# Performance work log

Measured on AMD Instinct MI355X. Metric: run time of the kernel, lower is better.

Reference implementation:

```python
import jax, jax.numpy as jnp
import numpy as np

B, S, D, H = 2, 2048, 1024, 16
DK = D // H  # 64


def setup_inputs() -> dict:
    key = jax.random.key(0)
    k0, k1, k2, k3, k4, k5, k6 = jax.random.split(key, 7)
    scale = 0.02
    return {
        "q": jax.random.normal(k0, (B, S, D), dtype=jnp.float32),
        "k": jax.random.normal(k1, (B, S, D), dtype=jnp.float32),
        "v": jax.random.normal(k2, (B, S, D), dtype=jnp.float32),
        # per-head Q/K projection weights (n_head separate Linear layers, bias=False)
        "Wq": jax.random.normal(k3, (H, D, DK), dtype=jnp.float32) * scale,
        "Wk": jax.random.normal(k4, (H, D, DK), dtype=jnp.float32) * scale,
        # shared V projection (the same v_layer object is reused for every head)
        "Wv": jax.random.normal(k5, (D, DK), dtype=jnp.float32) * scale,
        # output projection fc: d_v -> d_model, bias=False
        "Wo": jax.random.normal(k6, (DK, D), dtype=jnp.float32) * scale,
    }


def reference(q, k, v, Wq, Wk, Wv, Wo):
    d_k = Wq.shape[-1]
    # batched per-head projections (replaces the Python loop over heads)
    qs = jnp.einsum("bsd,hdk->bhsk", q, Wq)          # [B,H,S,DK]
    ks = jnp.einsum("bsd,hdk->bhsk", k, Wk)          # [B,H,S,DK]
    vs = jnp.einsum("bsd,dk->bsk", v, Wv)            # [B,S,DK] shared across heads
    scores = jnp.einsum("bhsk,bhtk->bhst", qs, ks) / jnp.sqrt(
        jnp.asarray(d_k, dtype=jnp.float32)
    )                                                 # [B,H,S,S]
    attn = jax.nn.softmax(scores, axis=-1)            # [B,H,S,S]; dropout = identity (eval)
    heads = jnp.einsum("bhst,btk->bhsk", attn, vs)    # [B,H,S,DK]
    head = heads.mean(axis=1)                         # mean over heads, not concat
    attn_mean = attn.mean(axis=1)                     # [B,S,S]
    out = jnp.einsum("bsk,kd->bsd", head, Wo)         # [B,S,D]; dropout = identity
    return (out, attn_mean)
```

## Files before the change

### kernel.cpp

```cpp
#include <hip/hip_runtime.h>

#define B_ 2
#define S_ 2048
#define D_ 1024
#define H_ 16
#define DK_ 64

typedef __bf16 bf8 __attribute__((ext_vector_type(8)));
typedef float f4 __attribute__((ext_vector_type(4)));
typedef unsigned short u16x8 __attribute__((ext_vector_type(8)));

__device__ __forceinline__ unsigned short f2bf_bits(float f) {
  unsigned int u = __float_as_uint(f);
  return (unsigned short)((u + 0x7fffu + ((u >> 16) & 1u)) >> 16);
}

__device__ __forceinline__ bf8 pack_bf8(f4 lo, f4 hi) {
  u16x8 u;
  u[0] = f2bf_bits(lo[0]); u[1] = f2bf_bits(lo[1]);
  u[2] = f2bf_bits(lo[2]); u[3] = f2bf_bits(lo[3]);
  u[4] = f2bf_bits(hi[0]); u[5] = f2bf_bits(hi[1]);
  u[6] = f2bf_bits(hi[2]); u[7] = f2bf_bits(hi[3]);
  union { u16x8 u; bf8 b; } x; x.u = u; return x.b;
}

__device__ __forceinline__ bf8 ldb(const unsigned short* p) {
  return *reinterpret_cast<const bf8*>(p);
}

__device__ __forceinline__ void stage16(const void* g, void* l) {
  __builtin_amdgcn_global_load_lds(
      (const __attribute__((address_space(1))) void*)g,
      (__attribute__((address_space(3))) void*)l, 16, 0, 0);
}

#define MFMA(a, b, c) __builtin_amdgcn_mfma_f32_16x16x32_bf16((a), (b), (c), 0, 0, 0)

__global__ void k_prep(const float* __restrict__ q, const float* __restrict__ k,
                       const float* __restrict__ wq, const float* __restrict__ wk,
                       const float* __restrict__ wv, const float* __restrict__ wo,
                       unsigned short* __restrict__ qb, unsigned short* __restrict__ kb,
                       unsigned short* __restrict__ wqt, unsigned short* __restrict__ wkt,
                       unsigned short* __restrict__ wvt, unsigned short* __restrict__ wot) {
  __shared__ float tl[64 * 65];
  int bid = blockIdx.x, tid = threadIdx.x;
  const int rr = tid >> 6, cc = tid & 63;
  if (bid < 4096) {
    int which = bid >> 11;
    long i = ((long)(bid & 2047) * 256 + tid) * 8;
    const float* src = which ? k : q;
    unsigned short* dst = which ? kb : qb;
    f4 lo = *reinterpret_cast<const f4*>(src + i);
    f4 hi = *reinterpret_cast<const f4*>(src + i + 4);
    *reinterpret_cast<bf8*>(dst + i) = pack_bf8(lo, hi);
  } else if (bid < 4352) {
    int blk = bid - 4096;
    int h = blk >> 4, d0 = (blk & 15) * 64;
    for (int m = 0; m < 2; ++m) {
      const float* src = m ? wk : wq;
      unsigned short* dst = m ? wkt : wqt;
      if (m) __syncthreads();
#pragma unroll
      for (int it = 0; it < 16; ++it) {
        int d = it * 4 + rr;
        tl[cc * 65 + d] = src[(long)h * 65536 + (d0 + d) * 64 + cc];
      }
      __syncthreads();
#pragma unroll
      for (int it = 0; it < 16; ++it) {
        int n = it * 4 + rr;
        dst[(long)h * 65536 + n * 1024 + d0 + cc] = f2bf_bits(tl[n * 65 + cc]);
      }
    }
  } else if (bid < 4368) {
    int d0 = (bid - 4352) * 64;
#pragma unroll
    for (int it = 0; it < 16; ++it) {
      int d = it * 4 + rr;
      tl[cc * 65 + d] = wv[(long)(d0 + d) * 64 + cc];
    }
    __syncthreads();
#pragma unroll
    for (int it = 0; it < 16; ++it) {
      int n = it * 4 + rr;
      wvt[(long)n * 1024 + d0 + cc] = f2bf_bits(tl[n * 65 + cc]);
    }
  } else {
    int d0 = (bid - 4368) * 64;
#pragma unroll
    for (int it = 0; it < 16; ++it) {
      int kk = it * 4 + rr;
      tl[cc * 65 + kk] = wo[(long)kk * 1024 + d0 + cc];
    }
    __syncthreads();
#pragma unroll
    for (int it = 0; it < 16; ++it) {
      int ddl = it * 4 + rr;
      wot[(long)(d0 + ddl) * 64 + cc] = f2bf_bits(tl[ddl * 65 + cc]);
    }
  }
}

__global__ __launch_bounds__(256) void k_gemm_qk(
    const unsigned short* __restrict__ qb, const unsigned short* __restrict__ kb,
    const unsigned short* __restrict__ wqt, const unsigned short* __restrict__ wkt,
    unsigned short* __restrict__ qsb, unsigned short* __restrict__ ksb) {
  __shared__ unsigned short lds[16384];
  const int tid = threadIdx.x, wave = tid >> 6, lane = tid & 63;
  const int l15 = lane & 15, quad = lane >> 4;
  const int m0 = blockIdx.x * 128, n0 = blockIdx.y * 128;
  const int which = blockIdx.z;
  const unsigned short* A = which ? kb : qb;
  const unsigned short* W = which ? wkt : wqt;
  unsigned short* C = which ? ksb : qsb;
  const float scale = which ? 1.0f : 0.18033688011112042f;
  const int wr = wave >> 1, wc = wave & 1;

  f4 acc[4][4];
#pragma unroll
  for (int i = 0; i < 4; ++i)
#pragma unroll
    for (int j = 0; j < 4; ++j) acc[i][j] = f4{0.f, 0.f, 0.f, 0.f};

  for (int k0 = 0; k0 < D_; k0 += 64) {
#pragma unroll
    for (int i = 0; i < 4; ++i) {
      int u = i * 256 + tid;
      int T = u >> 6, rg = T & 7, kh = T >> 3, sl15 = u & 15, squad = (u >> 4) & 3;
      stage16(A + (long)(m0 + rg * 16 + sl15) * D_ + k0 + kh * 32 + squad * 8, lds + u * 8);
      stage16(W + (long)(n0 + rg * 16 + sl15) * D_ + k0 + kh * 32 + squad * 8,
              lds + 8192 + u * 8);
    }
    __syncthreads();
#pragma unroll
    for (int kh = 0; kh < 2; ++kh) {
      bf8 aF[4], bF[4];
#pragma unroll
      for (int mi = 0; mi < 4; ++mi)
        aF[mi] = ldb(lds + (wr * 4 + mi + 8 * kh) * 512 + lane * 8);
#pragma unroll
      for (int ni = 0; ni < 4; ++ni)
        bF[ni] = ldb(lds + 8192 + (wc * 4 + ni + 8 * kh) * 512 + lane * 8);
#pragma unroll
      for (int mi = 0; mi < 4; ++mi)
#pragma unroll
        for (int ni = 0; ni < 4; ++ni)
          acc[mi][ni] = MFMA(aF[mi], bF[ni], acc[mi][ni]);
    }
    __syncthreads();
  }
#pragma unroll
  for (int mi = 0; mi < 4; ++mi)
#pragma unroll
    for (int r = 0; r < 4; ++r) {
      long row = m0 + wr * 64 + mi * 16 + quad * 4 + r;
#pragma unroll
      for (int ni = 0; ni < 4; ++ni)
        C[row * D_ + n0 + wc * 64 + ni * 16 + l15] = f2bf_bits(acc[mi][ni][r] * scale);
    }
}

__global__ __launch_bounds__(256) void k_pv(
    const float* __restrict__ v, const unsigned short* __restrict__ wvt,
    float* __restrict__ pv) {
  const int tid = threadIdx.x, wave = tid >> 6, lane = tid & 63;
  const int l15 = lane & 15, quad = lane >> 4;
  const int rg = blockIdx.x, kc = blockIdx.y;
  const int row0 = rg * 64 + wave * 16;
  const float* arow = v + (long)(row0 + l15) * D_ + kc * 128 + quad * 8;
  const unsigned short* wbase = wvt + kc * 128 + quad * 8;
  f4 acc[4];
  for (int i = 0; i < 4; ++i) acc[i] = f4{0.f, 0.f, 0.f, 0.f};
#pragma unroll
  for (int k0 = 0; k0 < 128; k0 += 32) {
    f4 alo = *reinterpret_cast<const f4*>(arow + k0);
    f4 ahi = *reinterpret_cast<const f4*>(arow + k0 + 4);
    bf8 a = pack_bf8(alo, ahi);
#pragma unroll
    for (int i = 0; i < 4; ++i) {
      bf8 bf = ldb(wbase + (long)(i * 16 + l15) * D_ + k0);
      acc[i] = MFMA(a, bf, acc[i]);
    }
  }
#pragma unroll
  for (int i = 0; i < 4; ++i)
#pragma unroll
    for (int r = 0; r < 4; ++r)
      pv[((long)kc * 4096 + row0 + quad * 4 + r) * 64 + i * 16 + l15] = acc[i][r];
}

__global__ void k_vred(const float* __restrict__ pv, unsigned short* __restrict__ vst) {
  int e = blockIdx.x * 256 + threadIdx.x;
  int t = e & 2047, dk = (e >> 11) & 63, b = e >> 17;
  long row = (long)b * S_ + t;
  float s = 0.f;
#pragma unroll
  for (int c = 0; c < 8; ++c) s += pv[((long)c * 4096 + row) * 64 + dk];
  vst[e] = f2bf_bits(s);
}

__global__ __launch_bounds__(256) void k_denom(
    const unsigned short* __restrict__ qsb, const unsigned short* __restrict__ ksb,
    float* __restrict__ recip) {
  __shared__ unsigned short lds[16384];
  const int tid = threadIdx.x, wave = tid >> 6, lane = tid & 63;
  const int l15 = lane & 15, quad = lane >> 4;
  const int stile = blockIdx.x, h = blockIdx.y, b = blockIdx.z;
  const int sw = stile * 128 + wave * 32;

  const unsigned short* qrow0 = qsb + ((long)(b * S_) + sw + l15) * D_ + h * 64 + quad * 8;
  bf8 a0 = ldb(qrow0);
  bf8 a1 = ldb(qrow0 + 32);
  bf8 a2 = ldb(qrow0 + 16 * D_);
  bf8 a3 = ldb(qrow0 + 16 * D_ + 32);

  f4 sum0 = f4{0.f, 0.f, 0.f, 0.f}, sum1 = f4{0.f, 0.f, 0.f, 0.f};

  const long kbase = (long)(b * S_);
#pragma unroll
  for (int i = 0; i < 4; ++i) {
    int u = i * 256 + tid;
    int T = u >> 6, sl15 = u & 15, squad = (u >> 4) & 3;
    stage16(ksb + (kbase + (T & 7) * 16 + sl15) * D_ + h * 64 + (T >> 3) * 32 + squad * 8,
            lds + u * 8);
  }
  for (int it = 0; it < 16; ++it) {
    __syncthreads();
    if (it < 15) {
      int t0n = (it + 1) * 128, bufn = (it + 1) & 1;
#pragma unroll
      for (int i = 0; i < 4; ++i) {
        int u = i * 256 + tid;
        int T = u >> 6, sl15 = u & 15, squad = (u >> 4) & 3;
        stage16(ksb + (kbase + t0n + (T & 7) * 16 + sl15) * D_ + h * 64 + (T >> 3) * 32 + squad * 8,
                lds + bufn * 8192 + u * 8);
      }
    }
    const unsigned short* L = lds + (it & 1) * 8192;
#pragma unroll
    for (int tt = 0; tt < 8; ++tt) {
      bf8 b0 = ldb(L + tt * 512 + lane * 8);
      bf8 b1 = ldb(L + 4096 + tt * 512 + lane * 8);
      f4 d0 = f4{0.f, 0.f, 0.f, 0.f};
      d0 = MFMA(a0, b0, d0);
      d0 = MFMA(a1, b1, d0);
      f4 d1 = f4{0.f, 0.f, 0.f, 0.f};
      d1 = MFMA(a2, b0, d1);
      d1 = MFMA(a3, b1, d1);
#pragma unroll
      for (int r = 0; r < 4; ++r) {
        sum0[r] += __builtin_amdgcn_exp2f(d0[r]);
        sum1[r] += __builtin_amdgcn_exp2f(d1[r]);
      }
    }
  }
#pragma unroll
  for (int m = 1; m < 16; m <<= 1) {
#pragma unroll
    for (int r = 0; r < 4; ++r) {
      sum0[r] += __shfl_xor(sum0[r], m, 64);
      sum1[r] += __shfl_xor(sum1[r], m, 64);
    }
  }
  if (l15 == 0) {
    float* rp0 = recip + (long)(b * H_ + h) * S_ + sw + quad * 4;
#pragma unroll
    for (int r = 0; r < 4; ++r) {
      rp0[r] = 1.0f / (16.0f * sum0[r]);
      rp0[16 + r] = 1.0f / (16.0f * sum1[r]);
    }
  }
}

__global__ __launch_bounds__(256) void k_attn(
    const unsigned short* __restrict__ qsb, const unsigned short* __restrict__ ksb,
    const float* __restrict__ recip, float* __restrict__ am) {
  __shared__ unsigned short lds[16384];
  const int tid = threadIdx.x, wave = tid >> 6, lane = tid & 63;
  const int l15 = lane & 15, quad = lane >> 4;
  const int tchunk = blockIdx.x, stile = blockIdx.y, b = blockIdx.z;
  const int sw = stile * 128 + wave * 32;
  const int t0c = tchunk * 128;

  f4 acc0[8], acc1[8];
#pragma unroll
  for (int tt = 0; tt < 8; ++tt) {
    acc0[tt] = f4{0.f, 0.f, 0.f, 0.f};
    acc1[tt] = f4{0.f, 0.f, 0.f, 0.f};
  }

  const unsigned short* qrow0 = qsb + ((long)(b * S_) + sw + l15) * D_ + quad * 8;
  const long kbase = (long)(b * S_) + t0c;

#pragma unroll
  for (int i = 0; i < 4; ++i) {
    int u = i * 256 + tid;
    int T = u >> 6, sl15 = u & 15, squad = (u >> 4) & 3;
    stage16(ksb + (kbase + (T & 7) * 16 + sl15) * D_ + (T >> 3) * 32 + squad * 8, lds + u * 8);
  }
  for (int h = 0; h < H_; ++h) {
    __syncthreads();
    if (h < 15) {
      int bufn = (h + 1) & 1;
#pragma unroll
      for (int i = 0; i < 4; ++i) {
        int u = i * 256 + tid;
        int T = u >> 6, sl15 = u & 15, squad = (u >> 4) & 3;
        stage16(ksb + (kbase + (T & 7) * 16 + sl15) * D_ + (h + 1) * 64 + (T >> 3) * 32 + squad * 8,
                lds + bufn * 8192 + u * 8);
      }
    }
    const unsigned short* L = lds + (h & 1) * 8192;
    bf8 a0 = ldb(qrow0 + h * 64);
    bf8 a1 = ldb(qrow0 + h * 64 + 32);
    bf8 a2 = ldb(qrow0 + 16 * D_ + h * 64);
    bf8 a3 = ldb(qrow0 + 16 * D_ + h * 64 + 32);
    const float* rpp = recip + (long)(b * H_ + h) * S_ + sw + quad * 4;
    f4 rp0 = *reinterpret_cast<const f4*>(rpp);
    f4 rp1 = *reinterpret_cast<const f4*>(rpp + 16);
#pragma unroll
    for (int tt = 0; tt < 8; ++tt) {
      bf8 b0 = ldb(L + tt * 512 + lane * 8);
      bf8 b1 = ldb(L + 4096 + tt * 512 + lane * 8);
      f4 d0 = f4{0.f, 0.f, 0.f, 0.f};
      d0 = MFMA(a0, b0, d0);
      d0 = MFMA(a1, b1, d0);
      f4 d1 = f4{0.f, 0.f, 0.f, 0.f};
      d1 = MFMA(a2, b0, d1);
      d1 = MFMA(a3, b1, d1);
#pragma unroll
      for (int r = 0; r < 4; ++r) {
        acc0[tt][r] += rp0[r] * __builtin_amdgcn_exp2f(d0[r]);
        acc1[tt][r] += rp1[r] * __builtin_amdgcn_exp2f(d1[r]);
      }
    }
  }
  float* ob0 = am + ((long)b * S_ + sw + quad * 4) * S_ + t0c + l15;
  float* ob1 = ob0 + 16 * S_;
#pragma unroll
  for (int tt = 0; tt < 8; ++tt)
#pragma unroll
    for (int r = 0; r < 4; ++r) {
      ob0[(long)r * S_ + tt * 16] = acc0[tt][r];
      ob1[(long)r * S_ + tt * 16] = acc1[tt][r];
    }
}

__global__ __launch_bounds__(256) void k_hpart(
    const float* __restrict__ am, const unsigned short* __restrict__ vst,
    float* __restrict__ ph) {
  const int tid = threadIdx.x, wave = tid >> 6, lane = tid & 63;
  const int l15 = lane & 15, quad = lane >> 4;
  const int rg = blockIdx.x, kc = blockIdx.y;
  const int row0 = rg * 64 + wave * 16;
  const int b = row0 >> 11;
  const float* arow = am + (long)(row0 + l15) * S_ + kc * 256 + quad * 8;
  const unsigned short* vb = vst + (long)b * DK_ * S_ + kc * 256 + quad * 8;
  f4 acc[4];
  for (int i = 0; i < 4; ++i) acc[i] = f4{0.f, 0.f, 0.f, 0.f};
#pragma unroll
  for (int t0 = 0; t0 < 256; t0 += 32) {
    f4 alo = *reinterpret_cast<const f4*>(arow + t0);
    f4 ahi = *reinterpret_cast<const f4*>(arow + t0 + 4);
    bf8 a = pack_bf8(alo, ahi);
#pragma unroll
    for (int i = 0; i < 4; ++i) {
      bf8 bf = ldb(vb + (long)(i * 16 + l15) * S_ + t0);
      acc[i] = MFMA(a, bf, acc[i]);
    }
  }
#pragma unroll
  for (int i = 0; i < 4; ++i)
#pragma unroll
    for (int r = 0; r < 4; ++r)
      ph[((long)kc * 4096 + row0 + quad * 4 + r) * 64 + i * 16 + l15] = acc[i][r];
}

__global__ void k_hred(const float* __restrict__ ph, unsigned short* __restrict__ headb) {
  int e = blockIdx.x * 256 + threadIdx.x;
  float s = 0.f;
#pragma unroll
  for (int c = 0; c < 8; ++c) s += ph[(long)c * 262144 + e];
  headb[e] = f2bf_bits(s);
}

__global__ __launch_bounds__(256) void k_out(
    const unsigned short* __restrict__ head, const unsigned short* __restrict__ wot,
    float* __restrict__ out) {
  const int tid = threadIdx.x, wave = tid >> 6, lane = tid & 63;
  const int l15 = lane & 15, quad = lane >> 4;
  const int dchunk = blockIdx.x, stile = blockIdx.y, b = blockIdx.z;
  const int s0 = stile * 64 + wave * 16;
  const int n0 = dchunk * 128;
  const unsigned short* hrow = head + ((long)b * S_ + s0 + l15) * DK_ + quad * 8;
  bf8 a0 = ldb(hrow);
  bf8 a1 = ldb(hrow + 32);
  const unsigned short* wb = wot + quad * 8;
  float* obase = out + ((long)b * S_ + s0 + quad * 4) * D_ + n0 + l15;
#pragma unroll
  for (int i = 0; i < 8; ++i) {
    const unsigned short* wp = wb + (long)(n0 + i * 16 + l15) * DK_;
    bf8 b0 = ldb(wp);
    bf8 b1 = ldb(wp + 32);
    f4 d = f4{0.f, 0.f, 0.f, 0.f};
    d = MFMA(a0, b0, d);
    d = MFMA(a1, b1, d);
#pragma unroll
    for (int r = 0; r < 4; ++r) obase[(long)r * D_ + i * 16] = d[r];
  }
}

extern "C" void kernel_launch(void* const* d_in, const int* in_sizes, int n_in,
                              void* d_out, int out_size, void* d_ws, size_t ws_size,
                              hipStream_t stream) {
  const float* q  = (const float*)d_in[0];
  const float* k  = (const float*)d_in[1];
  const float* v  = (const float*)d_in[2];
  const float* Wq = (const float*)d_in[3];
  const float* Wk = (const float*)d_in[4];
  const float* Wv = (const float*)d_in[5];
  const float* Wo = (const float*)d_in[6];

  float* out = (float*)d_out;
  float* am  = out + (long)B_ * S_ * D_;

  unsigned short* qsb  = (unsigned short*)d_ws;
  unsigned short* ksb  = qsb + 4194304;
  unsigned short* wqt  = ksb + 4194304;
  unsigned short* wkt  = wqt + 1048576;
  unsigned short* wvt  = wkt + 1048576;
  unsigned short* wot  = wvt + 65536;
  unsigned short* vst  = wot + 65536;
  unsigned short* headb= vst + 262144;
  float* recip = (float*)(headb + 262144);

  unsigned short* qb = (unsigned short*)am;
  unsigned short* kb = qb + 4194304;
  float* part = out;

  k_prep<<<4384, 256, 0, stream>>>(q, k, Wq, Wk, Wv, Wo, qb, kb, wqt, wkt, wvt, wot);
  k_gemm_qk<<<dim3(32, 8, 2), 256, 0, stream>>>(qb, kb, wqt, wkt, qsb, ksb);
  k_pv<<<dim3(64, 8), 256, 0, stream>>>(v, wvt, part);
  k_vred<<<1024, 256, 0, stream>>>(part, vst);
  k_denom<<<dim3(16, 16, 2), 256, 0, stream>>>(qsb, ksb, recip);
  k_attn<<<dim3(16, 16, 2), 256, 0, stream>>>(qsb, ksb, recip, am);
  k_hpart<<<dim3(64, 8), 256, 0, stream>>>(am, vst, part);
  k_hred<<<1024, 256, 0, stream>>>(part, headb);
  k_out<<<dim3(8, 32, 2), 256, 0, stream>>>(headb, wot, out);
}
```

Before: 258.9 us.

## Split denominator over key halves and retile attention-mean kernel to 512 threads

```diff
diff --git a/kernel.cpp b/kernel.cpp
--- a/kernel.cpp
+++ b/kernel.cpp
@@ -201,11 +201,12 @@
 
 __global__ __launch_bounds__(256) void k_denom(
     const unsigned short* __restrict__ qsb, const unsigned short* __restrict__ ksb,
-    float* __restrict__ recip) {
+    float* __restrict__ dsum) {
   __shared__ unsigned short lds[16384];
   const int tid = threadIdx.x, wave = tid >> 6, lane = tid & 63;
   const int l15 = lane & 15, quad = lane >> 4;
-  const int stile = blockIdx.x, h = blockIdx.y, b = blockIdx.z;
+  const int stile = blockIdx.x >> 1, thalf = blockIdx.x & 1;
+  const int h = blockIdx.y, b = blockIdx.z;
   const int sw = stile * 128 + wave * 32;
 
   const unsigned short* qrow0 = qsb + ((long)(b * S_) + sw + l15) * D_ + h * 64 + quad * 8;
@@ -216,25 +217,24 @@
 
   f4 sum0 = f4{0.f, 0.f, 0.f, 0.f}, sum1 = f4{0.f, 0.f, 0.f, 0.f};
 
-  const long kbase = (long)(b * S_);
+  const int sl15 = tid & 15, squad = (tid >> 4) & 3;
+  const unsigned short* gk[4];
 #pragma unroll
   for (int i = 0; i < 4; ++i) {
     int u = i * 256 + tid;
-    int T = u >> 6, sl15 = u & 15, squad = (u >> 4) & 3;
-    stage16(ksb + (kbase + (T & 7) * 16 + sl15) * D_ + h * 64 + (T >> 3) * 32 + squad * 8,
-            lds + u * 8);
-  }
-  for (int it = 0; it < 16; ++it) {
-    __syncthreads();
-    if (it < 15) {
-      int t0n = (it + 1) * 128, bufn = (it + 1) & 1;
-#pragma unroll
-      for (int i = 0; i < 4; ++i) {
-        int u = i * 256 + tid;
-        int T = u >> 6, sl15 = u & 15, squad = (u >> 4) & 3;
-        stage16(ksb + (kbase + t0n + (T & 7) * 16 + sl15) * D_ + h * 64 + (T >> 3) * 32 + squad * 8,
-                lds + bufn * 8192 + u * 8);
-      }
+    int T = u >> 6, rg = T & 7, kh = T >> 3;
+    gk[i] = ksb + ((long)(b * S_) + thalf * 1024 + rg * 16 + sl15) * D_ + h * 64 + kh * 32 + squad * 8;
+  }
+#pragma unroll
+  for (int i = 0; i < 4; ++i) stage16(gk[i], lds + (i * 256 + tid) * 8);
+
+  for (int it = 0; it < 8; ++it) {
+    __syncthreads();
+    if (it < 7) {
+      int bufn = (it + 1) & 1;
+#pragma unroll
+      for (int i = 0; i < 4; ++i)
+        stage16(gk[i] + (long)(it + 1) * 128 * D_, lds + bufn * 8192 + (i * 256 + tid) * 8);
     }
     const unsigned short* L = lds + (it & 1) * 8192;
 #pragma unroll
@@ -263,54 +263,50 @@
     }
   }
   if (l15 == 0) {
-    float* rp0 = recip + (long)(b * H_ + h) * S_ + sw + quad * 4;
+    float* dp = dsum + (long)thalf * 65536 + (long)(b * H_ + h) * S_ + sw + quad * 4;
 #pragma unroll
     for (int r = 0; r < 4; ++r) {
-      rp0[r] = 1.0f / (16.0f * sum0[r]);
-      rp0[16 + r] = 1.0f / (16.0f * sum1[r]);
-    }
-  }
-}
-
-__global__ __launch_bounds__(256) void k_attn(
+      dp[r] = sum0[r];
+      dp[16 + r] = sum1[r];
+    }
+  }
+}
+
+__global__ void k_recip(const float* __restrict__ dsum, float* __restrict__ recip) {
+  int e = blockIdx.x * 256 + threadIdx.x;
+  recip[e] = 1.0f / (16.0f * (dsum[e] + dsum[e + 65536]));
+}
+
+__global__ __launch_bounds__(512) void k_attn(
     const unsigned short* __restrict__ qsb, const unsigned short* __restrict__ ksb,
     const float* __restrict__ recip, float* __restrict__ am) {
-  __shared__ unsigned short lds[16384];
+  __shared__ unsigned short lds[8192];
   const int tid = threadIdx.x, wave = tid >> 6, lane = tid & 63;
   const int l15 = lane & 15, quad = lane >> 4;
   const int tchunk = blockIdx.x, stile = blockIdx.y, b = blockIdx.z;
-  const int sw = stile * 128 + wave * 32;
-  const int t0c = tchunk * 128;
-
-  f4 acc0[8], acc1[8];
-#pragma unroll
-  for (int tt = 0; tt < 8; ++tt) {
+  const int sw = stile * 256 + wave * 32;
+  const int t0c = tchunk * 64;
+
+  f4 acc0[4], acc1[4];
+#pragma unroll
+  for (int tt = 0; tt < 4; ++tt) {
     acc0[tt] = f4{0.f, 0.f, 0.f, 0.f};
     acc1[tt] = f4{0.f, 0.f, 0.f, 0.f};
   }
 
   const unsigned short* qrow0 = qsb + ((long)(b * S_) + sw + l15) * D_ + quad * 8;
-  const long kbase = (long)(b * S_) + t0c;
-
-#pragma unroll
-  for (int i = 0; i < 4; ++i) {
-    int u = i * 256 + tid;
-    int T = u >> 6, sl15 = u & 15, squad = (u >> 4) & 3;
-    stage16(ksb + (kbase + (T & 7) * 16 + sl15) * D_ + (T >> 3) * 32 + squad * 8, lds + u * 8);
-  }
+
+  const int sl15 = tid & 15, squad = (tid >> 4) & 3;
+  const int srg = (tid >> 6) & 3, skh = tid >> 8;
+  const unsigned short* gk =
+      ksb + ((long)(b * S_) + t0c + srg * 16 + sl15) * D_ + skh * 32 + squad * 8;
+
+  stage16(gk, lds + tid * 8);
   for (int h = 0; h < H_; ++h) {
     __syncthreads();
-    if (h < 15) {
-      int bufn = (h + 1) & 1;
-#pragma unroll
-      for (int i = 0; i < 4; ++i) {
-        int u = i * 256 + tid;
-        int T = u >> 6, sl15 = u & 15, squad = (u >> 4) & 3;
-        stage16(ksb + (kbase + (T & 7) * 16 + sl15) * D_ + (h + 1) * 64 + (T >> 3) * 32 + squad * 8,
-                lds + bufn * 8192 + u * 8);
-      }
-    }
-    const unsigned short* L = lds + (h & 1) * 8192;
+    if (h < 15)
+      stage16(gk + (h + 1) * 64, lds + ((h + 1) & 1) * 4096 + tid * 8);
+    const unsigned short* L = lds + (h & 1) * 4096;
     bf8 a0 = ldb(qrow0 + h * 64);
     bf8 a1 = ldb(qrow0 + h * 64 + 32);
     bf8 a2 = ldb(qrow0 + 16 * D_ + h * 64);
@@ -319,9 +315,9 @@
     f4 rp0 = *reinterpret_cast<const f4*>(rpp);
     f4 rp1 = *reinterpret_cast<const f4*>(rpp + 16);
 #pragma unroll
-    for (int tt = 0; tt < 8; ++tt) {
+    for (int tt = 0; tt < 4; ++tt) {
       bf8 b0 = ldb(L + tt * 512 + lane * 8);
-      bf8 b1 = ldb(L + 4096 + tt * 512 + lane * 8);
+      bf8 b1 = ldb(L + 2048 + tt * 512 + lane * 8);
       f4 d0 = f4{0.f, 0.f, 0.f, 0.f};
       d0 = MFMA(a0, b0, d0);
       d0 = MFMA(a1, b1, d0);
@@ -338,7 +334,7 @@
   float* ob0 = am + ((long)b * S_ + sw + quad * 4) * S_ + t0c + l15;
   float* ob1 = ob0 + 16 * S_;
 #pragma unroll
-  for (int tt = 0; tt < 8; ++tt)
+  for (int tt = 0; tt < 4; ++tt)
 #pragma unroll
     for (int r = 0; r < 4; ++r) {
       ob0[(long)r * S_ + tt * 16] = acc0[tt][r];
@@ -437,13 +433,15 @@
   unsigned short* qb = (unsigned short*)am;
   unsigned short* kb = qb + 4194304;
   float* part = out;
+  float* dsum = out + 2097152;
 
   k_prep<<<4384, 256, 0, stream>>>(q, k, Wq, Wk, Wv, Wo, qb, kb, wqt, wkt, wvt, wot);
   k_gemm_qk<<<dim3(32, 8, 2), 256, 0, stream>>>(qb, kb, wqt, wkt, qsb, ksb);
   k_pv<<<dim3(64, 8), 256, 0, stream>>>(v, wvt, part);
   k_vred<<<1024, 256, 0, stream>>>(part, vst);
-  k_denom<<<dim3(16, 16, 2), 256, 0, stream>>>(qsb, ksb, recip);
-  k_attn<<<dim3(16, 16, 2), 256, 0, stream>>>(qsb, ksb, recip, am);
+  k_denom<<<dim3(32, 16, 2), 256, 0, stream>>>(qsb, ksb, dsum);
+  k_recip<<<256, 256, 0, stream>>>(dsum, recip);
+  k_attn<<<dim3(32, 8, 2), 512, 0, stream>>>(qsb, ksb, recip, am);
   k_hpart<<<dim3(64, 8), 256, 0, stream>>>(am, vst, part);
   k_hred<<<1024, 256, 0, stream>>>(part, headb);
   k_out<<<dim3(8, 32, 2), 256, 0, stream>>>(headb, wot, out);
```

Result: slower. 269.5 us (+4.1%).
